# Kernel optimization log

Measured on AMD Instinct MI355X. Metric: run time of the kernel, lower is better.

The kernel has to match this reference:

```python
import jax, jax.numpy as jnp
import numpy as np

B, T, C, H, L = 1024, 20, 512, 8, 8
V, BS = 2, 32
D = C // H
EPS = 1e-5


def setup_inputs() -> dict:
    key = jax.random.key(0)
    ks = iter(jax.random.split(key, 16))
    n = lambda shape, s=0.02: jax.random.normal(next(ks), shape, dtype=jnp.float32) * s
    return {
        "x": jax.random.normal(next(ks), (B, T, V), dtype=jnp.float32),
        "enc_w": n((V, C)), "enc_b": jnp.zeros((C,), jnp.float32),
        "wpe": n((BS, C)),
        "ln1_w": jnp.ones((L, C), jnp.float32), "ln1_b": jnp.zeros((L, C), jnp.float32),
        "attn_w": n((L, C, 3 * C)), "attn_b": jnp.zeros((L, 3 * C), jnp.float32),
        "proj_w": n((L, C, C), 0.02 / np.sqrt(2 * L)), "proj_b": jnp.zeros((L, C), jnp.float32),
        "ln2_w": jnp.ones((L, C), jnp.float32), "ln2_b": jnp.zeros((L, C), jnp.float32),
        "fc1_w": n((L, C, 4 * C)), "fc1_b": jnp.zeros((L, 4 * C), jnp.float32),
        "fc2_w": n((L, 4 * C, C), 0.02 / np.sqrt(2 * L)), "fc2_b": jnp.zeros((L, C), jnp.float32),
        "lnf_w": jnp.ones((C,), jnp.float32), "lnf_b": jnp.zeros((C,), jnp.float32),
        "pred_w": n((C, V)), "pred_b": jnp.zeros((V,), jnp.float32),
    }


def _ln(x, w, b):
    mu = x.mean(-1, keepdims=True)
    var = x.var(-1, keepdims=True)  # biased, matches torch LayerNorm
    return (x - mu) * jax.lax.rsqrt(var + EPS) * w + b


def _forward(x, enc_w, enc_b, wpe, ln1_w, ln1_b, attn_w, attn_b, proj_w, proj_b,
             ln2_w, ln2_b, fc1_w, fc1_b, fc2_w, fc2_b, lnf_w, lnf_b, pred_w, pred_b):
    # traj_encoder_1 + positional embeddings (pos = arange(1, T+1), T != 9)
    h = x @ enc_w + enc_b + wpe[1:T + 1]
    mask = jnp.tril(jnp.ones((T, T), bool))  # causal mask
    scale = 1.0 / np.sqrt(D)

    def block(h, p):
        l1w, l1b, aw, ab, pw, pb, l2w, l2b, f1w, f1b, f2w, f2b = p
        qkv = _ln(h, l1w, l1b) @ aw + ab          # [B,T,3C]
        q, k, v = jnp.split(qkv, 3, axis=-1)
        q = q.reshape(B, T, H, D).transpose(0, 2, 1, 3)
        k = k.reshape(B, T, H, D).transpose(0, 2, 1, 3)
        v = v.reshape(B, T, H, D).transpose(0, 2, 1, 3)
        att = jnp.einsum('bhqd,bhkd->bhqk', q, k) * scale
        att = jnp.where(mask, att, -jnp.inf)
        att = jax.nn.softmax(att, axis=-1)
        y = jnp.einsum('bhqk,bhkd->bhqd', att, v)
        y = y.transpose(0, 2, 1, 3).reshape(B, T, C)
        h = h + y @ pw + pb
        m = _ln(h, l2w, l2b)
        h = h + jax.nn.gelu(m @ f1w + f1b, approximate=False) @ f2w + f2b
        return h, None

    params = (ln1_w, ln1_b, attn_w, attn_b, proj_w, proj_b,
              ln2_w, ln2_b, fc1_w, fc1_b, fc2_w, fc2_b)
    h, _ = jax.lax.scan(block, h, params)
    feat = _ln(h, lnf_w, lnf_b)
    return feat @ pred_w + pred_b  # predictor_1 -> [B,T,2]


def reference(x, enc_w, enc_b, wpe, ln1_w, ln1_b, attn_w, attn_b, proj_w, proj_b,
              ln2_w, ln2_b, fc1_w, fc1_b, fc2_w, fc2_b, lnf_w, lnf_b, pred_w, pred_b):
    return _forward(x, enc_w, enc_b, wpe, ln1_w, ln1_b, attn_w, attn_b, proj_w, proj_b,
                    ln2_w, ln2_b, fc1_w, fc1_b, fc2_w, fc2_b, lnf_w, lnf_b, pred_w, pred_b)
```

## Files before the change

kernel.cpp:

```cpp
#include <hip/hip_runtime.h>
#include <hip/hip_bf16.h>
#include <math.h>

#define NB 1024
#define NT 20
#define NC 512
#define NH 8
#define NL 8
#define MTOK (NB*NT)

using bf16 = __hip_bfloat16;
typedef float f32x4 __attribute__((ext_vector_type(4)));
typedef short s16x8 __attribute__((ext_vector_type(8)));

static __device__ __forceinline__ float us2f(unsigned short u) {
    union { float f; unsigned int i; } c; c.i = ((unsigned int)u) << 16; return c.f;
}
static __device__ __forceinline__ unsigned short f2bfu(float x) {
    union { bf16 b; unsigned short u; } c; c.b = __float2bfloat16(x); return c.u;
}
static __device__ __forceinline__ bf16 f2bf(float x) { return __float2bfloat16(x); }

static __device__ __forceinline__ void cp16(const bf16* g, bf16* lds_base, int lane) {
#if __has_builtin(__builtin_amdgcn_global_load_lds)
    __builtin_amdgcn_global_load_lds(
        (const __attribute__((address_space(1))) unsigned int*)g,
        (__attribute__((address_space(3))) unsigned int*)lds_base, 16, 0, 0);
#else
    ((int4*)lds_base)[lane] = *(const int4*)g;
#endif
}

__global__ __launch_bounds__(256) void enc_kernel(
    const float* __restrict__ x, const float* __restrict__ ew,
    const float* __restrict__ eb, const float* __restrict__ wpe,
    float* __restrict__ h) {
    int idx = blockIdx.x * 256 + threadIdx.x;
    int token = idx >> 7, c4 = idx & 127;
    int t = token % NT;
    float x0 = x[(size_t)token * 2], x1 = x[(size_t)token * 2 + 1];
    const float4* w4 = (const float4*)ew;
    float4 w0 = w4[c4], w1 = w4[128 + c4];
    float4 b = ((const float4*)eb)[c4];
    float4 pe = ((const float4*)(wpe + (size_t)(t + 1) * NC))[c4];
    float4 o;
    o.x = x0 * w0.x + x1 * w1.x + b.x + pe.x;
    o.y = x0 * w0.y + x1 * w1.y + b.y + pe.y;
    o.z = x0 * w0.z + x1 * w1.z + b.z + pe.z;
    o.w = x0 * w0.w + x1 * w1.w + b.w + pe.w;
    ((float4*)h)[idx] = o;
}

__global__ __launch_bounds__(256) void wconv_kernel(
    const float* __restrict__ in, bf16* __restrict__ out, int K, int N) {
    __shared__ float tile[32][33];
    int z = blockIdx.z;
    int k0 = blockIdx.x * 32, n0 = blockIdx.y * 32;
    int tx = threadIdx.x & 31, ty = threadIdx.x >> 5;
    const float* src = in + (size_t)z * K * N;
    bf16* dst = out + (size_t)z * K * N;
#pragma unroll
    for (int i = 0; i < 4; ++i)
        tile[ty + i * 8][tx] = src[(size_t)(k0 + ty + i * 8) * N + n0 + tx];
    __syncthreads();
#pragma unroll
    for (int i = 0; i < 4; ++i)
        dst[(size_t)(n0 + ty + i * 8) * K + k0 + tx] = f2bf(tile[tx][ty + i * 8]);
}

__global__ __launch_bounds__(256) void ln_kernel(
    const float* __restrict__ h, const float* __restrict__ w,
    const float* __restrict__ b, bf16* __restrict__ out) {
    int lane = threadIdx.x & 63, wave = threadIdx.x >> 6;
    int token = blockIdx.x * 4 + wave;
    const float4* row = (const float4*)(h + (size_t)token * NC);
    float4 v0 = row[lane], v1 = row[lane + 64];
    float s  = v0.x + v0.y + v0.z + v0.w + v1.x + v1.y + v1.z + v1.w;
    float sq = v0.x*v0.x + v0.y*v0.y + v0.z*v0.z + v0.w*v0.w
             + v1.x*v1.x + v1.y*v1.y + v1.z*v1.z + v1.w*v1.w;
#pragma unroll
    for (int off = 32; off; off >>= 1) {
        s  += __shfl_xor(s, off, 64);
        sq += __shfl_xor(sq, off, 64);
    }
    float mean = s * (1.0f / NC);
    float var = sq * (1.0f / NC) - mean * mean;
    float rstd = rsqrtf(var + 1e-5f);
    const float4* w4 = (const float4*)w;
    const float4* b4 = (const float4*)b;
    float4 wa = w4[lane], wb = w4[lane + 64];
    float4 ba = b4[lane], bb = b4[lane + 64];
    ushort4 o0, o1;
    o0.x = f2bfu((v0.x - mean) * rstd * wa.x + ba.x);
    o0.y = f2bfu((v0.y - mean) * rstd * wa.y + ba.y);
    o0.z = f2bfu((v0.z - mean) * rstd * wa.z + ba.z);
    o0.w = f2bfu((v0.w - mean) * rstd * wa.w + ba.w);
    o1.x = f2bfu((v1.x - mean) * rstd * wb.x + bb.x);
    o1.y = f2bfu((v1.y - mean) * rstd * wb.y + bb.y);
    o1.z = f2bfu((v1.z - mean) * rstd * wb.z + bb.z);
    o1.w = f2bfu((v1.w - mean) * rstd * wb.w + bb.w);
    *(ushort4*)(out + (size_t)token * NC + lane * 4) = o0;
    *(ushort4*)(out + (size_t)token * NC + 256 + lane * 4) = o1;
}

template <int EPI>
__global__ __launch_bounds__(256) void gemm(
    const bf16* __restrict__ A, const bf16* __restrict__ Wt,
    const float* __restrict__ bias, float* __restrict__ resid_out,
    bf16* __restrict__ outb, int N, int K) {
    __shared__ __align__(16) bf16 lA[128 * 32];
    __shared__ __align__(16) bf16 lB[128 * 32];
    const int tid = threadIdx.x;
    const int lane = tid & 63;
    const int wave = tid >> 6;
    const int wm = wave >> 1, wn = wave & 1;

    const int flat = blockIdx.y * gridDim.x + blockIdx.x;
    const int per = (gridDim.x * gridDim.y) >> 3;
    const int nid = (flat & 7) * per + (flat >> 3);
    const int mt = nid / gridDim.x;
    const int nt = nid - mt * gridDim.x;
    const int m0 = mt * 128, n0 = nt * 128;

    f32x4 acc[4][4] = {};

    const int c0 = tid, c1 = tid + 256;
    const int r0 = c0 >> 2, q0 = (c0 & 3) * 8;
    const int r1 = c1 >> 2, q1 = (c1 & 3) * 8;
    const bf16* Ab = A + (size_t)m0 * K;
    const bf16* Bb = Wt + (size_t)n0 * K;
    bf16* lA0 = lA + (wave * 64) * 8;
    bf16* lA1 = lA + (256 + wave * 64) * 8;
    bf16* lB0 = lB + (wave * 64) * 8;
    bf16* lB1 = lB + (256 + wave * 64) * 8;

    const int fm = lane & 15;
    const int fk = (lane >> 4) * 8;

    for (int k0 = 0; k0 < K; k0 += 32) {
        __syncthreads();
        cp16(Ab + (size_t)r0 * K + k0 + q0, lA0, lane);
        cp16(Ab + (size_t)r1 * K + k0 + q1, lA1, lane);
        cp16(Bb + (size_t)r0 * K + k0 + q0, lB0, lane);
        cp16(Bb + (size_t)r1 * K + k0 + q1, lB1, lane);
        __syncthreads();

        s16x8 af[4], bfr[4];
#pragma unroll
        for (int mi = 0; mi < 4; ++mi)
            af[mi] = *(const s16x8*)&lA[(wm * 64 + mi * 16 + fm) * 32 + fk];
#pragma unroll
        for (int ni = 0; ni < 4; ++ni)
            bfr[ni] = *(const s16x8*)&lB[(wn * 64 + ni * 16 + fm) * 32 + fk];
#pragma unroll
        for (int mi = 0; mi < 4; ++mi)
#pragma unroll
            for (int ni = 0; ni < 4; ++ni)
                acc[mi][ni] = __builtin_amdgcn_mfma_f32_16x16x32_bf16(
                    af[mi], bfr[ni], acc[mi][ni], 0, 0, 0);
    }

    const int er = lane >> 4;
    const int ec = lane & 15;
#pragma unroll
    for (int mi = 0; mi < 4; ++mi) {
#pragma unroll
        for (int ni = 0; ni < 4; ++ni) {
            int col = n0 + wn * 64 + ni * 16 + ec;
            float bcol = bias[col];
#pragma unroll
            for (int r = 0; r < 4; ++r) {
                int row = m0 + wm * 64 + mi * 16 + er * 4 + r;
                float v = acc[mi][ni][r] + bcol;
                size_t idx = (size_t)row * N + col;
                if (EPI == 0) {
                    outb[idx] = f2bf(v);
                } else if (EPI == 1) {
                    resid_out[idx] += v;
                } else {
                    float g = 0.5f * v * (1.0f + erff(v * 0.70710678118654752f));
                    outb[idx] = f2bf(g);
                }
            }
        }
    }
}

__global__ __launch_bounds__(64) void attn_kernel(
    const bf16* __restrict__ qkv, bf16* __restrict__ y) {
    __shared__ __align__(16) float qs[NT][68];
    __shared__ __align__(16) float ks[NT][68];
    __shared__ float vT[64][21];
    __shared__ __align__(16) float P[NT][24];
    const int lane = threadIdx.x;
    const int b = blockIdx.x >> 3, hh = blockIdx.x & 7;
    const bf16* base = qkv + (size_t)b * NT * (3 * NC) + hh * 64;

    for (int idx = lane; idx < NT * 32; idx += 64) {
        int t = idx >> 5, d2 = (idx & 31) * 2;
        const unsigned short* p;
        p = (const unsigned short*)(base + (size_t)t * (3 * NC) + d2);
        qs[t][d2] = us2f(p[0]); qs[t][d2 + 1] = us2f(p[1]);
        p = (const unsigned short*)(base + (size_t)t * (3 * NC) + NC + d2);
        ks[t][d2] = us2f(p[0]); ks[t][d2 + 1] = us2f(p[1]);
        p = (const unsigned short*)(base + (size_t)t * (3 * NC) + 2 * NC + d2);
        vT[d2][t] = us2f(p[0]); vT[d2 + 1][t] = us2f(p[1]);
    }
    __syncthreads();

    for (int pp = lane; pp < NT * NT; pp += 64) {
        int i = (int)(((unsigned)pp * 52429u) >> 20);
        int j = pp - i * 20;
        const float4* qi = (const float4*)qs[i];
        const float4* kj = (const float4*)ks[j];
        float s = 0.0f;
#pragma unroll
        for (int d4 = 0; d4 < 16; ++d4) {
            float4 a = qi[d4], c = kj[d4];
            s += a.x * c.x + a.y * c.y + a.z * c.z + a.w * c.w;
        }
        P[i][j] = s * 0.125f;
    }
    __syncthreads();

    if (lane < NT) {
        int i = lane;
        float m = -INFINITY;
        for (int j = 0; j <= i; ++j) m = fmaxf(m, P[i][j]);
        float sum = 0.0f;
        for (int j = 0; j <= i; ++j) { float e = __expf(P[i][j] - m); P[i][j] = e; sum += e; }
        float inv = 1.0f / sum;
        for (int j = 0; j <= i; ++j) P[i][j] *= inv;
        for (int j = i + 1; j < NT; ++j) P[i][j] = 0.0f;
    }
    __syncthreads();

    float vr[NT];
#pragma unroll
    for (int j = 0; j < NT; ++j) vr[j] = vT[lane][j];
    bf16* yb = y + (size_t)b * NT * NC + hh * 64;
#pragma unroll
    for (int i = 0; i < NT; ++i) {
        const float4* pr = (const float4*)P[i];
        float o = 0.0f;
#pragma unroll
        for (int j4 = 0; j4 < 5; ++j4) {
            float4 pv = pr[j4];
            o += pv.x * vr[j4 * 4] + pv.y * vr[j4 * 4 + 1]
               + pv.z * vr[j4 * 4 + 2] + pv.w * vr[j4 * 4 + 3];
        }
        yb[(size_t)i * NC + lane] = f2bf(o);
    }
}

__global__ __launch_bounds__(256) void lnf_pred_kernel(
    const float* __restrict__ h, const float* __restrict__ w,
    const float* __restrict__ b, const float* __restrict__ pw,
    const float* __restrict__ pb, float* __restrict__ out) {
    int lane = threadIdx.x & 63, wave = threadIdx.x >> 6;
    int token = blockIdx.x * 4 + wave;
    const float4* row = (const float4*)(h + (size_t)token * NC);
    float4 v0 = row[lane], v1 = row[lane + 64];
    float s  = v0.x + v0.y + v0.z + v0.w + v1.x + v1.y + v1.z + v1.w;
    float sq = v0.x*v0.x + v0.y*v0.y + v0.z*v0.z + v0.w*v0.w
             + v1.x*v1.x + v1.y*v1.y + v1.z*v1.z + v1.w*v1.w;
#pragma unroll
    for (int off = 32; off; off >>= 1) {
        s  += __shfl_xor(s, off, 64);
        sq += __shfl_xor(sq, off, 64);
    }
    float mean = s * (1.0f / NC);
    float var = sq * (1.0f / NC) - mean * mean;
    float rstd = rsqrtf(var + 1e-5f);
    const float4* w4 = (const float4*)w;
    const float4* b4 = (const float4*)b;
    float4 wa = w4[lane], wb = w4[lane + 64];
    float4 ba = b4[lane], bb = b4[lane + 64];
    const float2* pw2 = (const float2*)pw;
    float a0 = 0.0f, a1 = 0.0f;
    int c = lane * 4;
    float f; float2 pv;
    f = (v0.x - mean) * rstd * wa.x + ba.x; pv = pw2[c + 0]; a0 += f * pv.x; a1 += f * pv.y;
    f = (v0.y - mean) * rstd * wa.y + ba.y; pv = pw2[c + 1]; a0 += f * pv.x; a1 += f * pv.y;
    f = (v0.z - mean) * rstd * wa.z + ba.z; pv = pw2[c + 2]; a0 += f * pv.x; a1 += f * pv.y;
    f = (v0.w - mean) * rstd * wa.w + ba.w; pv = pw2[c + 3]; a0 += f * pv.x; a1 += f * pv.y;
    c = 256 + lane * 4;
    f = (v1.x - mean) * rstd * wb.x + bb.x; pv = pw2[c + 0]; a0 += f * pv.x; a1 += f * pv.y;
    f = (v1.y - mean) * rstd * wb.y + bb.y; pv = pw2[c + 1]; a0 += f * pv.x; a1 += f * pv.y;
    f = (v1.z - mean) * rstd * wb.z + bb.z; pv = pw2[c + 2]; a0 += f * pv.x; a1 += f * pv.y;
    f = (v1.w - mean) * rstd * wb.w + bb.w; pv = pw2[c + 3]; a0 += f * pv.x; a1 += f * pv.y;
#pragma unroll
    for (int off = 32; off; off >>= 1) {
        a0 += __shfl_xor(a0, off, 64);
        a1 += __shfl_xor(a1, off, 64);
    }
    if (lane == 0) {
        out[(size_t)token * 2]     = a0 + pb[0];
        out[(size_t)token * 2 + 1] = a1 + pb[1];
    }
}

extern "C" void kernel_launch(void* const* d_in, const int* in_sizes, int n_in,
                              void* d_out, int out_size, void* d_ws, size_t ws_size,
                              hipStream_t stream) {
    (void)in_sizes; (void)n_in; (void)out_size; (void)ws_size;
    const float* x      = (const float*)d_in[0];
    const float* enc_w  = (const float*)d_in[1];
    const float* enc_b  = (const float*)d_in[2];
    const float* wpe    = (const float*)d_in[3];
    const float* ln1_w  = (const float*)d_in[4];
    const float* ln1_b  = (const float*)d_in[5];
    const float* attn_w = (const float*)d_in[6];
    const float* attn_b = (const float*)d_in[7];
    const float* proj_w = (const float*)d_in[8];
    const float* proj_b = (const float*)d_in[9];
    const float* ln2_w  = (const float*)d_in[10];
    const float* ln2_b  = (const float*)d_in[11];
    const float* fc1_w  = (const float*)d_in[12];
    const float* fc1_b  = (const float*)d_in[13];
    const float* fc2_w  = (const float*)d_in[14];
    const float* fc2_b  = (const float*)d_in[15];
    const float* lnf_w  = (const float*)d_in[16];
    const float* lnf_b  = (const float*)d_in[17];
    const float* pred_w = (const float*)d_in[18];
    const float* pred_b = (const float*)d_in[19];
    float* out = (float*)d_out;

    char* p = (char*)d_ws;
    float* h  = (float*)p;  p += (size_t)MTOK * NC * 4;
    bf16* xa  = (bf16*)p;   p += (size_t)MTOK * NC * 2;
    bf16* big = (bf16*)p;   p += (size_t)MTOK * (4 * NC) * 2;
    bf16* aT  = (bf16*)p;   p += (size_t)NL * (3 * NC) * NC * 2;
    bf16* pT  = (bf16*)p;   p += (size_t)NL * NC * NC * 2;
    bf16* f1T = (bf16*)p;   p += (size_t)NL * (4 * NC) * NC * 2;
    bf16* f2T = (bf16*)p;   p += (size_t)NL * NC * (4 * NC) * 2;

    enc_kernel<<<MTOK * 128 / 256, 256, 0, stream>>>(x, enc_w, enc_b, wpe, h);
    wconv_kernel<<<dim3(16, 48, NL), 256, 0, stream>>>(attn_w, aT, NC, 3 * NC);
    wconv_kernel<<<dim3(16, 16, NL), 256, 0, stream>>>(proj_w, pT, NC, NC);
    wconv_kernel<<<dim3(16, 64, NL), 256, 0, stream>>>(fc1_w, f1T, NC, 4 * NC);
    wconv_kernel<<<dim3(64, 16, NL), 256, 0, stream>>>(fc2_w, f2T, 4 * NC, NC);

    for (int l = 0; l < NL; ++l) {
        ln_kernel<<<MTOK / 4, 256, 0, stream>>>(h, ln1_w + l * NC, ln1_b + l * NC, xa);
        gemm<0><<<dim3(12, 160), 256, 0, stream>>>(
            xa, aT + (size_t)l * 3 * NC * NC, attn_b + l * 3 * NC, nullptr, big, 3 * NC, NC);
        attn_kernel<<<NB * NH, 64, 0, stream>>>(big, xa);
        gemm<1><<<dim3(4, 160), 256, 0, stream>>>(
            xa, pT + (size_t)l * NC * NC, proj_b + l * NC, h, nullptr, NC, NC);
        ln_kernel<<<MTOK / 4, 256, 0, stream>>>(h, ln2_w + l * NC, ln2_b + l * NC, xa);
        gemm<2><<<dim3(16, 160), 256, 0, stream>>>(
            xa, f1T + (size_t)l * 4 * NC * NC, fc1_b + l * 4 * NC, nullptr, big, 4 * NC, NC);
        gemm<1><<<dim3(4, 160), 256, 0, stream>>>(
            big, f2T + (size_t)l * NC * 4 * NC, fc2_b + l * NC, h, nullptr, NC, 4 * NC);
    }
    lnf_pred_kernel<<<MTOK / 4, 256, 0, stream>>>(h, lnf_w, lnf_b, pred_w, pred_b, out);
}
```

Before: 2.762 ms.

## Swizzle GEMM LDS tiles, transpose MFMA output for vector stores, approximate GELU

XOR-swizzles the k-chunk placement of the A and B tiles in shared memory to reduce LDS bank conflicts on fragment reads. It swaps the MFMA operand order so each lane holds four consecutive columns, which lets the epilogue use vectorized bias loads, bf16x4 stores and float4 residual read-modify-writes instead of scalar strided accesses. It also replaces the exact erf GELU with the tanh approximation, written as x·sigmoid, using a fast exp and reciprocal. That approximation deviates slightly from the reference's exact GELU.

```diff
diff --git a/kernel.cpp b/kernel.cpp
--- a/kernel.cpp
+++ b/kernel.cpp
@@ -125,8 +125,8 @@
     f32x4 acc[4][4] = {};
 
     const int c0 = tid, c1 = tid + 256;
-    const int r0 = c0 >> 2, q0 = (c0 & 3) * 8;
-    const int r1 = c1 >> 2, q1 = (c1 & 3) * 8;
+    const int r0 = c0 >> 2, q0 = (((c0 & 3) ^ ((r0 >> 1) & 3)) * 8);
+    const int r1 = c1 >> 2, q1 = (((c1 & 3) ^ ((r1 >> 1) & 3)) * 8);
     const bf16* Ab = A + (size_t)m0 * K;
     const bf16* Bb = Wt + (size_t)n0 * K;
     bf16* lA0 = lA + (wave * 64) * 8;
@@ -135,7 +135,7 @@
     bf16* lB1 = lB + (256 + wave * 64) * 8;
 
     const int fm = lane & 15;
-    const int fk = (lane >> 4) * 8;
+    const int fk = (((lane >> 4) ^ ((fm >> 1) & 3)) * 8);
 
     for (int k0 = 0; k0 < K; k0 += 32) {
         __syncthreads();
@@ -157,30 +157,40 @@
 #pragma unroll
             for (int ni = 0; ni < 4; ++ni)
                 acc[mi][ni] = __builtin_amdgcn_mfma_f32_16x16x32_bf16(
-                    af[mi], bfr[ni], acc[mi][ni], 0, 0, 0);
+                    bfr[ni], af[mi], acc[mi][ni], 0, 0, 0);
     }
 
     const int er = lane >> 4;
     const int ec = lane & 15;
+    float4 bc[4];
+#pragma unroll
+    for (int ni = 0; ni < 4; ++ni)
+        bc[ni] = *(const float4*)&bias[n0 + wn * 64 + ni * 16 + er * 4];
 #pragma unroll
     for (int mi = 0; mi < 4; ++mi) {
+        int row = m0 + wm * 64 + mi * 16 + ec;
 #pragma unroll
         for (int ni = 0; ni < 4; ++ni) {
-            int col = n0 + wn * 64 + ni * 16 + ec;
-            float bcol = bias[col];
-#pragma unroll
-            for (int r = 0; r < 4; ++r) {
-                int row = m0 + wm * 64 + mi * 16 + er * 4 + r;
-                float v = acc[mi][ni][r] + bcol;
-                size_t idx = (size_t)row * N + col;
-                if (EPI == 0) {
-                    outb[idx] = f2bf(v);
-                } else if (EPI == 1) {
-                    resid_out[idx] += v;
-                } else {
-                    float g = 0.5f * v * (1.0f + erff(v * 0.70710678118654752f));
-                    outb[idx] = f2bf(g);
-                }
+            int colb = n0 + wn * 64 + ni * 16 + er * 4;
+            size_t idx = (size_t)row * N + colb;
+            float v0 = acc[mi][ni][0] + bc[ni].x;
+            float v1 = acc[mi][ni][1] + bc[ni].y;
+            float v2 = acc[mi][ni][2] + bc[ni].z;
+            float v3 = acc[mi][ni][3] + bc[ni].w;
+            if (EPI == 0) {
+                ushort4 o = { f2bfu(v0), f2bfu(v1), f2bfu(v2), f2bfu(v3) };
+                *(ushort4*)&outb[idx] = o;
+            } else if (EPI == 1) {
+                float4 old = *(const float4*)&resid_out[idx];
+                float4 nw = { old.x + v0, old.y + v1, old.z + v2, old.w + v3 };
+                *(float4*)&resid_out[idx] = nw;
+            } else {
+                float g0 = v0 * __builtin_amdgcn_rcpf(1.0f + __expf(-1.5957691f * v0 * (1.0f + 0.044715f * v0 * v0)));
+                float g1 = v1 * __builtin_amdgcn_rcpf(1.0f + __expf(-1.5957691f * v1 * (1.0f + 0.044715f * v1 * v1)));
+                float g2 = v2 * __builtin_amdgcn_rcpf(1.0f + __expf(-1.5957691f * v2 * (1.0f + 0.044715f * v2 * v2)));
+                float g3 = v3 * __builtin_amdgcn_rcpf(1.0f + __expf(-1.5957691f * v3 * (1.0f + 0.044715f * v3 * v3)));
+                ushort4 o = { f2bfu(g0), f2bfu(g1), f2bfu(g2), f2bfu(g3) };
+                *(ushort4*)&outb[idx] = o;
             }
         }
     }
```

Measured after the change: 2.920 ms. 1.06x slower.

## Double-buffer GEMM LDS with swizzle, add 128x64 tile kernel, fast GELU

Applied to the files above, without the earlier changes.

GEMM tiles are double-buffered in LDS: the next K-slice is issued with async global-to-LDS loads before computing the current one, and a partial vmcnt wait replaces the full sync. LDS addresses are XOR-swizzled to reduce bank conflicts on fragment reads. A 128x64 tile variant is added for the N=512 projection and fc2 GEMMs to double block count and improve occupancy. The erf GELU is replaced with a sigmoid-based tanh approximation, which changes numerics slightly.

```diff
diff --git a/kernel.cpp b/kernel.cpp
--- a/kernel.cpp
+++ b/kernel.cpp
@@ -29,6 +29,17 @@
 #else
     ((int4*)lds_base)[lane] = *(const int4*)g;
 #endif
+}
+
+static __device__ __forceinline__ void sync_sched() {
+#if __has_builtin(__builtin_amdgcn_sched_barrier)
+    __builtin_amdgcn_sched_barrier(0);
+#endif
+}
+
+static __device__ __forceinline__ float gelu_f(float v) {
+    return v * __builtin_amdgcn_rcpf(
+        1.0f + __expf(-1.5957691f * v * (1.0f + 0.044715f * v * v)));
 }
 
 __global__ __launch_bounds__(256) void enc_kernel(
@@ -108,8 +119,8 @@
     const bf16* __restrict__ A, const bf16* __restrict__ Wt,
     const float* __restrict__ bias, float* __restrict__ resid_out,
     bf16* __restrict__ outb, int N, int K) {
-    __shared__ __align__(16) bf16 lA[128 * 32];
-    __shared__ __align__(16) bf16 lB[128 * 32];
+    __shared__ __align__(16) bf16 lA[2][128 * 32];
+    __shared__ __align__(16) bf16 lB[2][128 * 32];
     const int tid = threadIdx.x;
     const int lane = tid & 63;
     const int wave = tid >> 6;
@@ -125,33 +136,38 @@
     f32x4 acc[4][4] = {};
 
     const int c0 = tid, c1 = tid + 256;
-    const int r0 = c0 >> 2, q0 = (c0 & 3) * 8;
-    const int r1 = c1 >> 2, q1 = (c1 & 3) * 8;
+    const int r0 = c0 >> 2, q0 = (((c0 & 3) ^ ((r0 >> 1) & 3)) * 8);
+    const int r1 = c1 >> 2, q1 = (((c1 & 3) ^ ((r1 >> 1) & 3)) * 8);
     const bf16* Ab = A + (size_t)m0 * K;
     const bf16* Bb = Wt + (size_t)n0 * K;
-    bf16* lA0 = lA + (wave * 64) * 8;
-    bf16* lA1 = lA + (256 + wave * 64) * 8;
-    bf16* lB0 = lB + (wave * 64) * 8;
-    bf16* lB1 = lB + (256 + wave * 64) * 8;
 
     const int fm = lane & 15;
-    const int fk = (lane >> 4) * 8;
-
-    for (int k0 = 0; k0 < K; k0 += 32) {
-        __syncthreads();
-        cp16(Ab + (size_t)r0 * K + k0 + q0, lA0, lane);
-        cp16(Ab + (size_t)r1 * K + k0 + q1, lA1, lane);
-        cp16(Bb + (size_t)r0 * K + k0 + q0, lB0, lane);
-        cp16(Bb + (size_t)r1 * K + k0 + q1, lB1, lane);
-        __syncthreads();
+    const int fk = (((lane >> 4) ^ ((fm >> 1) & 3)) * 8);
+    const int iters = K / 32;
+
+    auto stage = [&](int kk, int buf) {
+        cp16(Ab + (size_t)r0 * K + kk + q0, &lA[buf][(wave * 64) * 8], lane);
+        cp16(Ab + (size_t)r1 * K + kk + q1, &lA[buf][(256 + wave * 64) * 8], lane);
+        cp16(Bb + (size_t)r0 * K + kk + q0, &lB[buf][(wave * 64) * 8], lane);
+        cp16(Bb + (size_t)r1 * K + kk + q1, &lB[buf][(256 + wave * 64) * 8], lane);
+    };
+    stage(0, 0);
+    for (int it = 0; it < iters; ++it) {
+        const int cur = it & 1;
+        const int kn = (it + 1 < iters) ? (it + 1) * 32 : 0;
+        __builtin_amdgcn_s_barrier();
+        stage(kn, cur ^ 1);
+        __builtin_amdgcn_s_waitcnt(0xF74);
+        __builtin_amdgcn_s_barrier();
+        sync_sched();
 
         s16x8 af[4], bfr[4];
 #pragma unroll
         for (int mi = 0; mi < 4; ++mi)
-            af[mi] = *(const s16x8*)&lA[(wm * 64 + mi * 16 + fm) * 32 + fk];
+            af[mi] = *(const s16x8*)&lA[cur][(wm * 64 + mi * 16 + fm) * 32 + fk];
 #pragma unroll
         for (int ni = 0; ni < 4; ++ni)
-            bfr[ni] = *(const s16x8*)&lB[(wn * 64 + ni * 16 + fm) * 32 + fk];
+            bfr[ni] = *(const s16x8*)&lB[cur][(wn * 64 + ni * 16 + fm) * 32 + fk];
 #pragma unroll
         for (int mi = 0; mi < 4; ++mi)
 #pragma unroll
@@ -178,8 +194,92 @@
                 } else if (EPI == 1) {
                     resid_out[idx] += v;
                 } else {
-                    float g = 0.5f * v * (1.0f + erff(v * 0.70710678118654752f));
-                    outb[idx] = f2bf(g);
+                    outb[idx] = f2bf(gelu_f(v));
+                }
+            }
+        }
+    }
+}
+
+template <int EPI>
+__global__ __launch_bounds__(256) void gemm64(
+    const bf16* __restrict__ A, const bf16* __restrict__ Wt,
+    const float* __restrict__ bias, float* __restrict__ resid_out,
+    bf16* __restrict__ outb, int N, int K) {
+    __shared__ __align__(16) bf16 lA[2][128 * 32];
+    __shared__ __align__(16) bf16 lB[2][64 * 32];
+    const int tid = threadIdx.x;
+    const int lane = tid & 63;
+    const int wave = tid >> 6;
+
+    const int flat = blockIdx.y * gridDim.x + blockIdx.x;
+    const int per = (gridDim.x * gridDim.y) >> 3;
+    const int nid = (flat & 7) * per + (flat >> 3);
+    const int mt = nid / gridDim.x;
+    const int nt = nid - mt * gridDim.x;
+    const int m0 = mt * 128, n0 = nt * 64;
+
+    f32x4 acc[2][4] = {};
+
+    const int c0 = tid, c1 = tid + 256;
+    const int r0 = c0 >> 2, q0 = (((c0 & 3) ^ ((r0 >> 1) & 3)) * 8);
+    const int r1 = c1 >> 2, q1 = (((c1 & 3) ^ ((r1 >> 1) & 3)) * 8);
+    const bf16* Ab = A + (size_t)m0 * K;
+    const bf16* Bb = Wt + (size_t)n0 * K;
+
+    const int fm = lane & 15;
+    const int fk = (((lane >> 4) ^ ((fm >> 1) & 3)) * 8);
+    const int iters = K / 32;
+
+    auto stage = [&](int kk, int buf) {
+        cp16(Ab + (size_t)r0 * K + kk + q0, &lA[buf][(wave * 64) * 8], lane);
+        cp16(Ab + (size_t)r1 * K + kk + q1, &lA[buf][(256 + wave * 64) * 8], lane);
+        cp16(Bb + (size_t)r0 * K + kk + q0, &lB[buf][(wave * 64) * 8], lane);
+    };
+    stage(0, 0);
+    for (int it = 0; it < iters; ++it) {
+        const int cur = it & 1;
+        const int kn = (it + 1 < iters) ? (it + 1) * 32 : 0;
+        __builtin_amdgcn_s_barrier();
+        stage(kn, cur ^ 1);
+        __builtin_amdgcn_s_waitcnt(0xF73);
+        __builtin_amdgcn_s_barrier();
+        sync_sched();
+
+        s16x8 af[2], bfr[4];
+#pragma unroll
+        for (int mi = 0; mi < 2; ++mi)
+            af[mi] = *(const s16x8*)&lA[cur][(wave * 32 + mi * 16 + fm) * 32 + fk];
+#pragma unroll
+        for (int ni = 0; ni < 4; ++ni)
+            bfr[ni] = *(const s16x8*)&lB[cur][(ni * 16 + fm) * 32 + fk];
+#pragma unroll
+        for (int mi = 0; mi < 2; ++mi)
+#pragma unroll
+            for (int ni = 0; ni < 4; ++ni)
+                acc[mi][ni] = __builtin_amdgcn_mfma_f32_16x16x32_bf16(
+                    af[mi], bfr[ni], acc[mi][ni], 0, 0, 0);
+    }
+
+    const int er = lane >> 4;
+    const int ec = lane & 15;
+#pragma unroll
+    for (int mi = 0; mi < 2; ++mi) {
+#pragma unroll
+        for (int ni = 0; ni < 4; ++ni) {
+            int col = n0 + ni * 16 + ec;
+            float bcol = bias[col];
+#pragma unroll
+            for (int r = 0; r < 4; ++r) {
+                int row = m0 + wave * 32 + mi * 16 + er * 4 + r;
+                float v = acc[mi][ni][r] + bcol;
+                size_t idx = (size_t)row * N + col;
+                if (EPI == 0) {
+                    outb[idx] = f2bf(v);
+                } else if (EPI == 1) {
+                    resid_out[idx] += v;
+                } else {
+                    outb[idx] = f2bf(gelu_f(v));
                 }
             }
         }
@@ -346,12 +446,12 @@
         gemm<0><<<dim3(12, 160), 256, 0, stream>>>(
             xa, aT + (size_t)l * 3 * NC * NC, attn_b + l * 3 * NC, nullptr, big, 3 * NC, NC);
         attn_kernel<<<NB * NH, 64, 0, stream>>>(big, xa);
-        gemm<1><<<dim3(4, 160), 256, 0, stream>>>(
+        gemm64<1><<<dim3(8, 160), 256, 0, stream>>>(
             xa, pT + (size_t)l * NC * NC, proj_b + l * NC, h, nullptr, NC, NC);
         ln_kernel<<<MTOK / 4, 256, 0, stream>>>(h, ln2_w + l * NC, ln2_b + l * NC, xa);
         gemm<2><<<dim3(16, 160), 256, 0, stream>>>(
             xa, f1T + (size_t)l * 4 * NC * NC, fc1_b + l * 4 * NC, nullptr, big, 4 * NC, NC);
-        gemm<1><<<dim3(4, 160), 256, 0, stream>>>(
+        gemm64<1><<<dim3(8, 160), 256, 0, stream>>>(
             big, f2T + (size_t)l * NC * 4 * NC, fc2_b + l * NC, h, nullptr, NC, 4 * NC);
     }
     lnf_pred_kernel<<<MTOK / 4, 256, 0, stream>>>(h, lnf_w, lnf_b, pred_w, pred_b, out);
```

Measured after the change: 2.539 ms. 8.1% less time.
